# Kernel optimization log

Measured on AMD Instinct MI355X. Metric: run time of the kernel, lower is better.

## Reference

```python
import jax, jax.numpy as jnp
import numpy as np

N_NODES = 20000
DIM = 128
N_EDGES = 500000
BATCH = 16384
EPS = 1e-6  # torch.nn.PairwiseDistance default eps


def setup_inputs() -> dict:
    key = jax.random.key(0)
    k = jax.random.split(key, 8)
    edges = jax.random.randint(k[0], (2, N_EDGES), 0, N_NODES, dtype=jnp.int64 if jax.config.jax_enable_x64 else jnp.int32)
    nodes_p_star = jnp.sort(jax.random.randint(k[1], (BATCH,), 0, N_NODES))
    nodes_p = jnp.sort(jax.random.randint(k[2], (BATCH,), 0, N_NODES))
    # learned parameters, init in [-1, 1) as in the torch module
    beta_p = 2.0 * jax.random.uniform(k[3], (N_NODES,), dtype=jnp.float32) - 1.0
    beta_p_star = 2.0 * jax.random.uniform(k[4], (N_NODES,), dtype=jnp.float32) - 1.0
    p = 2.0 * jax.random.uniform(k[5], (N_NODES, DIM), dtype=jnp.float32) - 1.0
    p_star = 2.0 * jax.random.uniform(k[6], (N_NODES, DIM), dtype=jnp.float32) - 1.0
    return {
        "edges": edges,
        "nodes_p_star": nodes_p_star,
        "nodes_p": nodes_p,
        "beta_p": beta_p,
        "beta_p_star": beta_p_star,
        "p": p,
        "p_star": p_star,
    }


def reference(edges, nodes_p_star, nodes_p, beta_p, beta_p_star, p, p_star):
    # ---- link term: sum over observed edges of (beta - dist) ----
    beta_pair = beta_p_star[edges[0]] + beta_p[edges[1]]  # [E]
    diff = p[edges[0]] - p_star[edges[1]]                 # [E, D]
    # torch PairwiseDistance adds eps to the difference before the norm
    z_dist = jnp.sqrt(jnp.sum((diff + EPS) ** 2, axis=-1))
    link_term = jnp.sum(beta_pair - z_dist)

    # ---- non-link term: triu-masked sum of exp(beta - cdist) ----
    bps = beta_p_star[nodes_p_star]   # [Ns]
    bp = beta_p[nodes_p]              # [Np]
    ps = p_star[nodes_p_star]         # [Ns, D]
    pp = p[nodes_p]                   # [Np, D]
    beta_mat = bps[None, :] + bp[:, None]          # [Np, Ns]
    # cdist(ps, pp) -> [Ns, Np] via Gram trick
    sq = (jnp.sum(ps * ps, axis=-1)[:, None]
          + jnp.sum(pp * pp, axis=-1)[None, :]
          - 2.0 * jnp.einsum('nd,md->nm', ps, pp))
    dist_mat = jnp.sqrt(jnp.maximum(sq, 0.0))      # [Ns, Np]
    intensity = jnp.exp(beta_mat.T - dist_mat)     # [Ns, Np]
    non_link = jnp.sum(jnp.triu(intensity, k=1))

    return -(link_term - non_link)
```

## Files before the change

kernel.cpp:

```cpp
#include <hip/hip_runtime.h>

#define N_NODES 20000
#define DIM 128
#define N_EDGES 500000
#define BATCH 16384
#define EPS 1e-6f
#define L2E 1.4426950408889634f

typedef _Float16 half8 __attribute__((ext_vector_type(8)));
typedef _Float16 half4_t __attribute__((ext_vector_type(4)));
typedef float f32x4 __attribute__((ext_vector_type(4)));

__device__ __forceinline__ float fast_sqrtf(float x) {
#if __has_builtin(__builtin_amdgcn_sqrtf)
    return __builtin_amdgcn_sqrtf(x);
#else
    return sqrtf(x);
#endif
}
__device__ __forceinline__ float fast_exp2f(float x) {
#if __has_builtin(__builtin_amdgcn_exp2f)
    return __builtin_amdgcn_exp2f(x);
#else
    return exp2f(x);
#endif
}

#define NB_TILE 8256

#define OFF_PGEMM 0
#define OFF_PSH   33280
#define OFF_PPH   4227584
#define OFF_N2S   8421888
#define OFF_N2P   8487424
#define OFF_BPS   8552960
#define OFF_BP    8618496
#define OFF_END   8684032

__global__ __launch_bounds__(256) void prep_kernel(
    const float* __restrict__ p, const float* __restrict__ p_star,
    const float* __restrict__ beta_p, const float* __restrict__ beta_ps,
    const int* __restrict__ nodes_ps, const int* __restrict__ nodes_p,
    _Float16* __restrict__ Ah, float* __restrict__ n2A, float* __restrict__ bA2,
    _Float16* __restrict__ Bh, float* __restrict__ n2B, float* __restrict__ bB2)
{
    const int bx = blockIdx.x;
    const int g = threadIdx.x & 31;
    const int r8 = threadIdx.x >> 5;
    const bool isA = bx < 2048;
    const int row = (isA ? bx : bx - 2048) * 8 + r8;
    const int id = isA ? nodes_ps[row] : nodes_p[row];
    const float* src = isA ? p_star : p;
    float4 v = ((const float4*)(src + (size_t)id * DIM))[g];
    half4_t o;
    o[0] = (_Float16)v.x; o[1] = (_Float16)v.y; o[2] = (_Float16)v.z; o[3] = (_Float16)v.w;
    const int h = g >> 4;
    const int pc = ((g >> 1) & 7) ^ (row & 7);
    _Float16* dst = isA ? Ah : Bh;
    *(half4_t*)(dst + (size_t)row * DIM + (((h << 3) | pc) << 3) + (g & 1) * 4) = o;
    float nrm = v.x * v.x + v.y * v.y + v.z * v.z + v.w * v.w;
    #pragma unroll
    for (int m = 16; m >= 1; m >>= 1) nrm += __shfl_xor(nrm, m, 32);
    if (g == 0) {
        if (isA) { n2A[row] = nrm; bA2[row] = L2E * beta_ps[id]; }
        else     { n2B[row] = nrm; bB2[row] = L2E * beta_p[id]; }
    }
}

#define STAGE(h)                                                                   \
    {                                                                              \
        _Pragma("unroll")                                                          \
        for (int u = 0; u < 2; ++u) {                                              \
            const int cidx = w * 128 + u * 64 + lane;                              \
            const int row = cidx >> 3, cc = cidx & 7;                              \
            const int ldsoff = (w * 128 + u * 64) * 16;                            \
            __builtin_amdgcn_global_load_lds(                                      \
                (const __attribute__((address_space(1))) void*)(gA +               \
                    (((size_t)(i0 + row)) << 8) + ((h) << 7) + (cc << 4)),         \
                (__attribute__((address_space(3))) void*)(ldsA + ldsoff), 16, 0, 0); \
            __builtin_amdgcn_global_load_lds(                                      \
                (const __attribute__((address_space(1))) void*)(gB +               \
                    (((size_t)(j0 + row)) << 8) + ((h) << 7) + (cc << 4)),         \
                (__attribute__((address_space(3))) void*)(ldsB + ldsoff), 16, 0, 0); \
        }                                                                          \
    }

#define COMPUTE_HALF                                                               \
    if (cls != 2) {                                                                \
        _Pragma("unroll")                                                          \
        for (int ks = 0; ks < 2; ++ks) {                                           \
            const int lc = ks * 4 + quad;                                          \
            const int pcx = (lc ^ k7) << 3;                                        \
            half8 af[2], bf[4];                                                    \
            _Pragma("unroll")                                                      \
            for (int u = 0; u < 2; ++u)                                            \
                af[u] = *(const half8*)&As[(wm * 32 + u * 16 + lr) * 64 + pcx];    \
            _Pragma("unroll")                                                      \
            for (int v = 0; v < 4; ++v)                                            \
                bf[v] = *(const half8*)&Bs[(wn * 64 + v * 16 + lr) * 64 + pcx];    \
            _Pragma("unroll")                                                      \
            for (int mi = 0; mi < 2; ++mi)                                         \
                _Pragma("unroll")                                                  \
                for (int ni = 0; ni < 4; ++ni)                                     \
                    acc[mi][ni] = __builtin_amdgcn_mfma_f32_16x16x32_f16(          \
                        af[mi], bf[ni], acc[mi][ni], 0, 0, 0);                     \
        }                                                                          \
    }

__global__ __launch_bounds__(512, 4) void main_kernel(
    const _Float16* __restrict__ Ag, const _Float16* __restrict__ Bg,
    const float* __restrict__ n2A, const float* __restrict__ n2B,
    const float* __restrict__ bA2, const float* __restrict__ bB2,
    const int* __restrict__ edges,
    const float* __restrict__ beta_p, const float* __restrict__ beta_ps,
    const float* __restrict__ pf, const float* __restrict__ psf,
    float* __restrict__ pgemm)
{
    const int bx = blockIdx.x, by = blockIdx.y;
    int ti, tj;
    const int len = 128 - by;
    if (bx < len) { ti = by; tj = by + bx; }
    else          { ti = 127 - by; tj = 127 - (bx - len); }
    const int i0 = ti * 128, j0 = tj * 128;
    const int bid = by * 129 + bx;
    const bool diag = (ti == tj);

    __shared__ __align__(16) _Float16 As[128 * 64];
    __shared__ __align__(16) _Float16 Bs[128 * 64];
    __shared__ float smr[8];

    const int tid = threadIdx.x;
    const int lane = tid & 63;
    const int w = tid >> 6;
    const int wm = w & 3;
    const int wn = w >> 2;
    const int quad = lane >> 4;
    const int lr = lane & 15;
    const int k7 = lr & 7;

    auto* ldsA = (__attribute__((address_space(3))) char*)As;
    auto* ldsB = (__attribute__((address_space(3))) char*)Bs;
    const auto* gA = (const __attribute__((address_space(1))) char*)Ag;
    const auto* gB = (const __attribute__((address_space(1))) char*)Bg;

    STAGE(0)

    float lsum = 0.f;
    #pragma unroll
    for (int t = 0; t < 2; ++t) {
        int e = bid * 64 + w * 8 + quad * 2 + t;
        if (e < N_EDGES) {
            int e0 = edges[e];
            int e1 = edges[N_EDGES + e];
            const float* ar = pf + (size_t)e0 * DIM + lr * 8;
            const float* br = psf + (size_t)e1 * DIM + lr * 8;
            f32x4 a0 = *(const f32x4*)ar;       f32x4 a1 = *(const f32x4*)(ar + 4);
            f32x4 b0 = *(const f32x4*)br;       f32x4 b1 = *(const f32x4*)(br + 4);
            float eb2 = (lr == 0) ? (beta_ps[e0] + beta_p[e1]) : 0.f;
            float s = 0.f;
            #pragma unroll
            for (int k = 0; k < 4; ++k) { float d = a0[k] - b0[k] + EPS; s = fmaf(d, d, s); }
            #pragma unroll
            for (int k = 0; k < 4; ++k) { float d = a1[k] - b1[k] + EPS; s = fmaf(d, d, s); }
            #pragma unroll
            for (int m = 8; m >= 1; m >>= 1) s += __shfl_xor(s, m, 16);
            if (lr == 0) lsum -= eb2 - fast_sqrtf(s);
        }
    }

    __syncthreads();

    int cls = 0;
    if (diag) cls = (wn == 0) ? (wm >= 2 ? 2 : 1) : (wm >= 2 ? 1 : 0);

    f32x4 acc[2][4] = {};

    COMPUTE_HALF
    __syncthreads();
    STAGE(1)
    __syncthreads();
    COMPUTE_HALF

    const int ilo = i0 + wm * 32, jlo = j0 + wn * 64;
    if (cls != 2) {
        f32x4 n2i[2], bi[2];
        #pragma unroll
        for (int mi = 0; mi < 2; ++mi) {
            n2i[mi] = *(const f32x4*)&n2A[ilo + mi * 16 + quad * 4];
            bi[mi]  = *(const f32x4*)&bA2[ilo + mi * 16 + quad * 4];
        }
        float n2j[4], bj[4];
        #pragma unroll
        for (int ni = 0; ni < 4; ++ni) {
            n2j[ni] = n2B[jlo + ni * 16 + lr];
            bj[ni]  = bB2[jlo + ni * 16 + lr];
        }

        if (cls == 0) {
            #pragma unroll
            for (int mi = 0; mi < 2; ++mi)
                #pragma unroll
                for (int ni = 0; ni < 4; ++ni) {
                    f32x4 d = acc[mi][ni];
                    #pragma unroll
                    for (int r = 0; r < 4; ++r) {
                        float tt = n2i[mi][r] + n2j[ni];
                        float sq = fmaxf(fmaf(d[r], -2.f, tt), 0.f);
                        float arg = fmaf(fast_sqrtf(sq), -L2E, bi[mi][r] + bj[ni]);
                        lsum += fast_exp2f(arg);
                    }
                }
        } else {
            #pragma unroll
            for (int mi = 0; mi < 2; ++mi)
                #pragma unroll
                for (int ni = 0; ni < 4; ++ni) {
                    f32x4 d = acc[mi][ni];
                    #pragma unroll
                    for (int r = 0; r < 4; ++r) {
                        int ig = ilo + mi * 16 + quad * 4 + r;
                        int jg = jlo + ni * 16 + lr;
                        float tt = n2i[mi][r] + n2j[ni];
                        float sq = fmaxf(fmaf(d[r], -2.f, tt), 0.f);
                        float arg = fmaf(fast_sqrtf(sq), -L2E, bi[mi][r] + bj[ni]);
                        float ex = fast_exp2f(arg);
                        if (jg > ig) lsum += ex;
                    }
                }
        }
    }

    #pragma unroll
    for (int m = 32; m >= 1; m >>= 1) lsum += __shfl_xor(lsum, m, 64);
    if (lane == 0) smr[w] = lsum;
    __syncthreads();
    if (tid == 0) {
        float t = 0.f;
        #pragma unroll
        for (int i = 0; i < 8; ++i) t += smr[i];
        pgemm[bid] = t;
    }
}

__global__ __launch_bounds__(1024) void reduce_kernel(
    const float* __restrict__ pg, float* __restrict__ out)
{
    float s = 0.f;
    for (int k = threadIdx.x; k < NB_TILE; k += 1024) s += pg[k];
    #pragma unroll
    for (int m = 32; m >= 1; m >>= 1) s += __shfl_xor(s, m, 64);
    __shared__ float sm[16];
    if ((threadIdx.x & 63) == 0) sm[threadIdx.x >> 6] = s;
    __syncthreads();
    if (threadIdx.x == 0) {
        float t = 0.f;
        #pragma unroll
        for (int i = 0; i < 16; ++i) t += sm[i];
        out[0] = t;
    }
}

extern "C" void kernel_launch(void* const* d_in, const int* in_sizes, int n_in,
                              void* d_out, int out_size, void* d_ws, size_t ws_size,
                              hipStream_t stream) {
    const int* edges = (const int*)d_in[0];
    const int* nodes_p_star = (const int*)d_in[1];
    const int* nodes_p = (const int*)d_in[2];
    const float* beta_p = (const float*)d_in[3];
    const float* beta_p_star = (const float*)d_in[4];
    const float* p = (const float*)d_in[5];
    const float* p_star = (const float*)d_in[6];

    char* ws = (char*)d_ws;
    float* pgemm = (float*)(ws + OFF_PGEMM);
    _Float16* psh = (_Float16*)(ws + OFF_PSH);
    _Float16* pph = (_Float16*)(ws + OFF_PPH);
    float* n2s = (float*)(ws + OFF_N2S);
    float* n2p = (float*)(ws + OFF_N2P);
    float* bps2 = (float*)(ws + OFF_BPS);
    float* bp2 = (float*)(ws + OFF_BP);

    prep_kernel<<<4096, 256, 0, stream>>>(
        p, p_star, beta_p, beta_p_star, nodes_p_star, nodes_p,
        psh, n2s, bps2, pph, n2p, bp2);

    main_kernel<<<dim3(129, 64), 512, 0, stream>>>(
        psh, pph, n2s, n2p, bps2, bp2,
        edges, beta_p, beta_p_star, p, p_star,
        pgemm);

    reduce_kernel<<<1, 1024, 0, stream>>>(pgemm, (float*)d_out);
}
```

Before: 205.7 us.

## Make main kernel persistent with full-K LDS staging and next-tile prefetch

Replaces the 8256-block grid with 512 persistent blocks that loop over triangular tiles. Each block stages the whole K=128 slice into LDS at once, then issues the async global-to-LDS load for its next tile before running the edge-term work and the exp/sqrt epilogue of the current tile. The aim is to hide load latency behind the epilogue and cut launch and tail costs. In exchange LDS use doubles, which may lower occupancy, and the fixed 512-block stride can leave work unevenly spread across blocks.

```diff
diff --git a/kernel.cpp b/kernel.cpp
--- a/kernel.cpp
+++ b/kernel.cpp
@@ -27,6 +27,7 @@
 }
 
 #define NB_TILE 8256
+#define N_BLK   512
 
 #define OFF_PGEMM 0
 #define OFF_PSH   33280
@@ -67,43 +68,31 @@
     }
 }
 
-#define STAGE(h)                                                                   \
+__device__ __forceinline__ void tile_of(int t, int& i0, int& j0, bool& diag) {
+    const int by = t / 129;
+    const int bx = t - by * 129;
+    const int len = 128 - by;
+    int ti, tj;
+    if (bx < len) { ti = by; tj = by + bx; }
+    else          { ti = 127 - by; tj = 127 - (bx - len); }
+    i0 = ti << 7; j0 = tj << 7; diag = (ti == tj);
+}
+
+#define STAGE(I0, J0)                                                              \
     {                                                                              \
         _Pragma("unroll")                                                          \
-        for (int u = 0; u < 2; ++u) {                                              \
-            const int cidx = w * 128 + u * 64 + lane;                              \
-            const int row = cidx >> 3, cc = cidx & 7;                              \
-            const int ldsoff = (w * 128 + u * 64) * 16;                            \
+        for (int u = 0; u < 4; ++u) {                                              \
+            const int cidx = u * 512 + tid;                                        \
+            const int row = cidx >> 4, cc = cidx & 15;                             \
+            const int ldsoff = (u * 512 + w * 64) * 16;                            \
             __builtin_amdgcn_global_load_lds(                                      \
                 (const __attribute__((address_space(1))) void*)(gA +               \
-                    (((size_t)(i0 + row)) << 8) + ((h) << 7) + (cc << 4)),         \
+                    (((size_t)((I0) + row)) << 8) + (cc << 4)),                    \
                 (__attribute__((address_space(3))) void*)(ldsA + ldsoff), 16, 0, 0); \
             __builtin_amdgcn_global_load_lds(                                      \
                 (const __attribute__((address_space(1))) void*)(gB +               \
-                    (((size_t)(j0 + row)) << 8) + ((h) << 7) + (cc << 4)),         \
+                    (((size_t)((J0) + row)) << 8) + (cc << 4)),                    \
                 (__attribute__((address_space(3))) void*)(ldsB + ldsoff), 16, 0, 0); \
-        }                                                                          \
-    }
-
-#define COMPUTE_HALF                                                               \
-    if (cls != 2) {                                                                \
-        _Pragma("unroll")                                                          \
-        for (int ks = 0; ks < 2; ++ks) {                                           \
-            const int lc = ks * 4 + quad;                                          \
-            const int pcx = (lc ^ k7) << 3;                                        \
-            half8 af[2], bf[4];                                                    \
-            _Pragma("unroll")                                                      \
-            for (int u = 0; u < 2; ++u)                                            \
-                af[u] = *(const half8*)&As[(wm * 32 + u * 16 + lr) * 64 + pcx];    \
-            _Pragma("unroll")                                                      \
-            for (int v = 0; v < 4; ++v)                                            \
-                bf[v] = *(const half8*)&Bs[(wn * 64 + v * 16 + lr) * 64 + pcx];    \
-            _Pragma("unroll")                                                      \
-            for (int mi = 0; mi < 2; ++mi)                                         \
-                _Pragma("unroll")                                                  \
-                for (int ni = 0; ni < 4; ++ni)                                     \
-                    acc[mi][ni] = __builtin_amdgcn_mfma_f32_16x16x32_f16(          \
-                        af[mi], bf[ni], acc[mi][ni], 0, 0, 0);                     \
         }                                                                          \
     }
 
@@ -116,19 +105,11 @@
     const float* __restrict__ pf, const float* __restrict__ psf,
     float* __restrict__ pgemm)
 {
-    const int bx = blockIdx.x, by = blockIdx.y;
-    int ti, tj;
-    const int len = 128 - by;
-    if (bx < len) { ti = by; tj = by + bx; }
-    else          { ti = 127 - by; tj = 127 - (bx - len); }
-    const int i0 = ti * 128, j0 = tj * 128;
-    const int bid = by * 129 + bx;
-    const bool diag = (ti == tj);
-
-    __shared__ __align__(16) _Float16 As[128 * 64];
-    __shared__ __align__(16) _Float16 Bs[128 * 64];
+    __shared__ __align__(16) _Float16 As[128 * 128];
+    __shared__ __align__(16) _Float16 Bs[128 * 128];
     __shared__ float smr[8];
 
+    const int b = blockIdx.x;
     const int tid = threadIdx.x;
     const int lane = tid & 63;
     const int w = tid >> 6;
@@ -143,91 +124,123 @@
     const auto* gA = (const __attribute__((address_space(1))) char*)Ag;
     const auto* gB = (const __attribute__((address_space(1))) char*)Bg;
 
-    STAGE(0)
-
     float lsum = 0.f;
-    #pragma unroll
-    for (int t = 0; t < 2; ++t) {
-        int e = bid * 64 + w * 8 + quad * 2 + t;
-        if (e < N_EDGES) {
-            int e0 = edges[e];
-            int e1 = edges[N_EDGES + e];
-            const float* ar = pf + (size_t)e0 * DIM + lr * 8;
-            const float* br = psf + (size_t)e1 * DIM + lr * 8;
-            f32x4 a0 = *(const f32x4*)ar;       f32x4 a1 = *(const f32x4*)(ar + 4);
-            f32x4 b0 = *(const f32x4*)br;       f32x4 b1 = *(const f32x4*)(br + 4);
-            float eb2 = (lr == 0) ? (beta_ps[e0] + beta_p[e1]) : 0.f;
-            float s = 0.f;
+
+    int t = b;
+    int i0, j0; bool diag;
+    tile_of(t, i0, j0, diag);
+    STAGE(i0, j0)
+    __syncthreads();
+
+    for (;;) {
+        int cls = 0;
+        if (diag) cls = (wn == 0) ? (wm >= 2 ? 2 : 1) : (wm >= 2 ? 1 : 0);
+
+        f32x4 acc[2][4] = {};
+        if (cls != 2) {
             #pragma unroll
-            for (int k = 0; k < 4; ++k) { float d = a0[k] - b0[k] + EPS; s = fmaf(d, d, s); }
+            for (int ks = 0; ks < 4; ++ks) {
+                const int lc = ks * 4 + quad;
+                const int pcx = ((lc & 8) | ((lc & 7) ^ k7)) << 3;
+                half8 af[2], bf[4];
+                #pragma unroll
+                for (int u = 0; u < 2; ++u)
+                    af[u] = *(const half8*)&As[(wm * 32 + u * 16 + lr) * 128 + pcx];
+                #pragma unroll
+                for (int v = 0; v < 4; ++v)
+                    bf[v] = *(const half8*)&Bs[(wn * 64 + v * 16 + lr) * 128 + pcx];
+                #pragma unroll
+                for (int mi = 0; mi < 2; ++mi)
+                    #pragma unroll
+                    for (int ni = 0; ni < 4; ++ni)
+                        acc[mi][ni] = __builtin_amdgcn_mfma_f32_16x16x32_f16(
+                            af[mi], bf[ni], acc[mi][ni], 0, 0, 0);
+            }
+        }
+
+        const int ilo = i0 + wm * 32, jlo = j0 + wn * 64;
+        const int tcur = t;
+        __syncthreads();
+
+        t += N_BLK;
+        const bool more = (t < NB_TILE);
+        if (more) {
+            tile_of(t, i0, j0, diag);
+            STAGE(i0, j0)
+        }
+
+        #pragma unroll
+        for (int tt = 0; tt < 2; ++tt) {
+            int e = tcur * 64 + w * 8 + quad * 2 + tt;
+            if (e < N_EDGES) {
+                int e0 = edges[e];
+                int e1 = edges[N_EDGES + e];
+                const float* ar = pf + (size_t)e0 * DIM + lr * 8;
+                const float* br = psf + (size_t)e1 * DIM + lr * 8;
+                f32x4 a0 = *(const f32x4*)ar;   f32x4 a1 = *(const f32x4*)(ar + 4);
+                f32x4 b0 = *(const f32x4*)br;   f32x4 b1 = *(const f32x4*)(br + 4);
+                float eb2 = (lr == 0) ? (beta_ps[e0] + beta_p[e1]) : 0.f;
+                float s = 0.f;
+                #pragma unroll
+                for (int k = 0; k < 4; ++k) { float d = a0[k] - b0[k] + EPS; s = fmaf(d, d, s); }
+                #pragma unroll
+                for (int k = 0; k < 4; ++k) { float d = a1[k] - b1[k] + EPS; s = fmaf(d, d, s); }
+                #pragma unroll
+                for (int m = 8; m >= 1; m >>= 1) s += __shfl_xor(s, m, 16);
+                if (lr == 0) lsum -= eb2 - fast_sqrtf(s);
+            }
+        }
+
+        if (cls != 2) {
+            f32x4 n2i[2], bi[2];
             #pragma unroll
-            for (int k = 0; k < 4; ++k) { float d = a1[k] - b1[k] + EPS; s = fmaf(d, d, s); }
+            for (int mi = 0; mi < 2; ++mi) {
+                n2i[mi] = *(const f32x4*)&n2A[ilo + mi * 16 + quad * 4];
+                bi[mi]  = *(const f32x4*)&bA2[ilo + mi * 16 + quad * 4];
+            }
+            float n2j[4], bj[4];
             #pragma unroll
-            for (int m = 8; m >= 1; m >>= 1) s += __shfl_xor(s, m, 16);
-            if (lr == 0) lsum -= eb2 - fast_sqrtf(s);
+            for (int ni = 0; ni < 4; ++ni) {
+                n2j[ni] = n2B[jlo + ni * 16 + lr];
+                bj[ni]  = bB2[jlo + ni * 16 + lr];
+            }
+
+            if (cls == 0) {
+                #pragma unroll
+                for (int mi = 0; mi < 2; ++mi)
+                    #pragma unroll
+                    for (int ni = 0; ni < 4; ++ni) {
+                        f32x4 d = acc[mi][ni];
+                        #pragma unroll
+                        for (int r = 0; r < 4; ++r) {
+                            float tt = n2i[mi][r] + n2j[ni];
+                            float sq = fmaxf(fmaf(d[r], -2.f, tt), 0.f);
+                            float arg = fmaf(fast_sqrtf(sq), -L2E, bi[mi][r] + bj[ni]);
+                            lsum += fast_exp2f(arg);
+                        }
+                    }
+            } else {
+                #pragma unroll
+                for (int mi = 0; mi < 2; ++mi)
+                    #pragma unroll
+                    for (int ni = 0; ni < 4; ++ni) {
+                        f32x4 d = acc[mi][ni];
+                        #pragma unroll
+                        for (int r = 0; r < 4; ++r) {
+                            int ig = ilo + mi * 16 + quad * 4 + r;
+                            int jg = jlo + ni * 16 + lr;
+                            float tt = n2i[mi][r] + n2j[ni];
+                            float sq = fmaxf(fmaf(d[r], -2.f, tt), 0.f);
+                            float arg = fmaf(fast_sqrtf(sq), -L2E, bi[mi][r] + bj[ni]);
+                            float ex = fast_exp2f(arg);
+                            if (jg > ig) lsum += ex;
+                        }
+                    }
+            }
         }
-    }
-
-    __syncthreads();
-
-    int cls = 0;
-    if (diag) cls = (wn == 0) ? (wm >= 2 ? 2 : 1) : (wm >= 2 ? 1 : 0);
-
-    f32x4 acc[2][4] = {};
-
-    COMPUTE_HALF
-    __syncthreads();
-    STAGE(1)
-    __syncthreads();
-    COMPUTE_HALF
-
-    const int ilo = i0 + wm * 32, jlo = j0 + wn * 64;
-    if (cls != 2) {
-        f32x4 n2i[2], bi[2];
-        #pragma unroll
-        for (int mi = 0; mi < 2; ++mi) {
-            n2i[mi] = *(const f32x4*)&n2A[ilo + mi * 16 + quad * 4];
-            bi[mi]  = *(const f32x4*)&bA2[ilo + mi * 16 + quad * 4];
-        }
-        float n2j[4], bj[4];
-        #pragma unroll
-        for (int ni = 0; ni < 4; ++ni) {
-            n2j[ni] = n2B[jlo + ni * 16 + lr];
-            bj[ni]  = bB2[jlo + ni * 16 + lr];
-        }
-
-        if (cls == 0) {
-            #pragma unroll
-            for (int mi = 0; mi < 2; ++mi)
-                #pragma unroll
-                for (int ni = 0; ni < 4; ++ni) {
-                    f32x4 d = acc[mi][ni];
-                    #pragma unroll
-                    for (int r = 0; r < 4; ++r) {
-                        float tt = n2i[mi][r] + n2j[ni];
-                        float sq = fmaxf(fmaf(d[r], -2.f, tt), 0.f);
-                        float arg = fmaf(fast_sqrtf(sq), -L2E, bi[mi][r] + bj[ni]);
-                        lsum += fast_exp2f(arg);
-                    }
-                }
-        } else {
-            #pragma unroll
-            for (int mi = 0; mi < 2; ++mi)
-                #pragma unroll
-                for (int ni = 0; ni < 4; ++ni) {
-                    f32x4 d = acc[mi][ni];
-                    #pragma unroll
-                    for (int r = 0; r < 4; ++r) {
-                        int ig = ilo + mi * 16 + quad * 4 + r;
-                        int jg = jlo + ni * 16 + lr;
-                        float tt = n2i[mi][r] + n2j[ni];
-                        float sq = fmaxf(fmaf(d[r], -2.f, tt), 0.f);
-                        float arg = fmaf(fast_sqrtf(sq), -L2E, bi[mi][r] + bj[ni]);
-                        float ex = fast_exp2f(arg);
-                        if (jg > ig) lsum += ex;
-                    }
-                }
-        }
+
+        if (!more) break;
+        __syncthreads();
     }
 
     #pragma unroll
@@ -235,10 +248,10 @@
     if (lane == 0) smr[w] = lsum;
     __syncthreads();
     if (tid == 0) {
-        float t = 0.f;
+        float s = 0.f;
         #pragma unroll
-        for (int i = 0; i < 8; ++i) t += smr[i];
-        pgemm[bid] = t;
+        for (int i = 0; i < 8; ++i) s += smr[i];
+        pgemm[b] = s;
     }
 }
 
@@ -246,7 +259,7 @@
     const float* __restrict__ pg, float* __restrict__ out)
 {
     float s = 0.f;
-    for (int k = threadIdx.x; k < NB_TILE; k += 1024) s += pg[k];
+    for (int k = threadIdx.x; k < N_BLK; k += 1024) s += pg[k];
     #pragma unroll
     for (int m = 32; m >= 1; m >>= 1) s += __shfl_xor(s, m, 64);
     __shared__ float sm[16];
@@ -284,7 +297,7 @@
         p, p_star, beta_p, beta_p_star, nodes_p_star, nodes_p,
         psh, n2s, bps2, pph, n2p, bp2);
 
-    main_kernel<<<dim3(129, 64), 512, 0, stream>>>(
+    main_kernel<<<N_BLK, 512, 0, stream>>>(
         psh, pph, n2s, n2p, bps2, bp2,
         edges, beta_p, beta_p_star, p, p_star,
         pgemm);
```

Result: faster. 193.3 us (-6.0%).
